# Performance work log

Measured on AMD Instinct MI355X. Metric: run time of the kernel, lower is better.

## Reference

```python
import jax, jax.numpy as jnp
import numpy as np

B, N, D = 8, 4096, 512
K = 1228  # int(4096 * 0.3)
N_CH = 2


def setup_inputs() -> dict:
    key = jax.random.key(0)
    ks = jax.random.split(key, 6)
    return {
        "agents_states": jax.random.normal(ks[0], (B, N, D), jnp.float32),
        "net": jax.random.normal(ks[1], (N_CH, N, N), jnp.float32) * (1.0 / np.sqrt(N)),
        "gate_w": jax.random.normal(ks[2], (N_CH, D, 2 * D), jnp.float32) * 0.02,
        "gate_b": jnp.zeros((N_CH, D), jnp.float32),
        "cand_w": jax.random.normal(ks[3], (N_CH, D, D), jnp.float32) * 0.02,
        "cand_b": jnp.zeros((N_CH, D), jnp.float32),
        "ln_g": jnp.ones((N_CH, D), jnp.float32),
        "ln_b": jnp.zeros((N_CH, D), jnp.float32),
        "channel_mix": jnp.ones((N_CH,), jnp.float32) / N_CH,
        "k": K,
    }


def _layer_norm(h, g, b, eps=1e-5):
    mu = h.mean(-1, keepdims=True)
    var = jnp.mean((h - mu) ** 2, axis=-1, keepdims=True)
    return (h - mu) * jax.lax.rsqrt(var + eps) * g + b


def _channel(x, net, gw, gb, cw, cb, lg, lb):
    # fixed-graph message passing: [N,N] @ [B,N,D]
    interaction = jnp.einsum('mn,bnd->bmd', net, x)
    candidate = jax.nn.gelu(interaction @ cw.T + cb, approximate=False)
    gate = jax.nn.sigmoid(jnp.concatenate([x, interaction], axis=-1) @ gw.T + gb)
    return _layer_norm(gate * candidate + (1.0 - gate) * x, lg, lb)


def reference(agents_states, net, gate_w, gate_b, cand_w, cand_b, ln_g, ln_b, channel_mix, k):
    w = jax.nn.softmax(channel_mix, axis=0)
    out = jnp.zeros_like(agents_states)
    for c in range(net.shape[0]):  # fixed small channel count
        out = out + w[c] * _channel(agents_states, net[c], gate_w[c], gate_b[c],
                                    cand_w[c], cand_b[c], ln_g[c], ln_b[c])
    # sparse top-k activation over agents
    energy = jnp.linalg.norm(out, axis=-1)               # [B, N]
    _, top_idx = jax.lax.top_k(energy, k)                # [B, k]
    mask = jnp.zeros_like(energy).at[jnp.arange(energy.shape[0])[:, None], top_idx].set(1.0)
    mask = mask * (out.shape[1] / k)
    return out * mask[..., None]
```

## Files before the change

### kernel.cpp

```cpp
#include <hip/hip_runtime.h>
#include <hip/hip_bf16.h>
#include <math.h>

#define BB 8
#define NN 4096
#define DD 512
#define SLAB 2048
#define SROWS (BB * SLAB)

typedef short bf16x8 __attribute__((ext_vector_type(8)));
typedef float f32x4 __attribute__((ext_vector_type(4)));

#define AS1 __attribute__((address_space(1)))
#define AS3 __attribute__((address_space(3)))

__device__ __forceinline__ void gload_lds16(const void* g, void* l) {
    __builtin_amdgcn_global_load_lds((const AS1 unsigned int*)g,
                                     (AS3 unsigned int*)l, 16, 0, 0);
}

__device__ __forceinline__ void split_bf16(float v, unsigned short& h, unsigned short& l) {
    __hip_bfloat16 bh = __float2bfloat16(v);
    float hf = __bfloat162float(bh);
    __hip_bfloat16 bl = __float2bfloat16(v - hf);
    h = *reinterpret_cast<unsigned short*>(&bh);
    l = *reinterpret_cast<unsigned short*>(&bl);
}

__global__ __launch_bounds__(256)
void conv_split(const float* __restrict__ src, unsigned short* __restrict__ hi,
                unsigned short* __restrict__ lo)
{
    const size_t i = (size_t)blockIdx.x * 256 + threadIdx.x;
    float4 v = ((const float4*)src)[i];
    ushort4 h, l;
    split_bf16(v.x, h.x, l.x);
    split_bf16(v.y, h.y, l.y);
    split_bf16(v.z, h.z, l.z);
    split_bf16(v.w, h.w, l.w);
    ((ushort4*)hi)[i] = h;
    ((ushort4*)lo)[i] = l;
}

__global__ __launch_bounds__(256)
void conv_w3(const float* __restrict__ cw, const float* __restrict__ gw,
             unsigned short* __restrict__ cwh, unsigned short* __restrict__ cwl,
             unsigned short* __restrict__ gxh, unsigned short* __restrict__ gxl,
             unsigned short* __restrict__ gih, unsigned short* __restrict__ gil)
{
    const int blk = blockIdx.x;
    const int i = (blk & 255) * 256 + threadIdx.x;
    const int n = i >> 7, kq = (i & 127) * 4;
    const float* src;
    unsigned short *oh, *ol;
    if (blk < 256)      { src = cw + (size_t)n * 512 + kq;        oh = cwh; ol = cwl; }
    else if (blk < 512) { src = gw + (size_t)n * 1024 + kq;       oh = gxh; ol = gxl; }
    else                { src = gw + (size_t)n * 1024 + 512 + kq; oh = gih; ol = gil; }
    float4 v = *(const float4*)src;
    ushort4 h, l;
    split_bf16(v.x, h.x, l.x);
    split_bf16(v.y, h.y, l.y);
    split_bf16(v.z, h.z, l.z);
    split_bf16(v.w, h.w, l.w);
    *(ushort4*)(oh + (size_t)n * 512 + kq) = h;
    *(ushort4*)(ol + (size_t)n * 512 + kq) = l;
}

__global__ __launch_bounds__(256)
void conv_xs(const float* __restrict__ x, int nbase,
             unsigned short* __restrict__ hi, unsigned short* __restrict__ lo)
{
    const size_t i = (size_t)blockIdx.x * 256 + threadIdx.x;
    const int r = (int)(i >> 7), kq = (int)(i & 127) * 4;
    const int b = r >> 11, ii = r & (SLAB - 1);
    float4 v = *(const float4*)(x + ((size_t)(b << 12) + nbase + ii) * DD + kq);
    ushort4 h, l;
    split_bf16(v.x, h.x, l.x);
    split_bf16(v.y, h.y, l.y);
    split_bf16(v.z, h.z, l.z);
    split_bf16(v.w, h.w, l.w);
    *(ushort4*)(hi + (size_t)r * DD + kq) = h;
    *(ushort4*)(lo + (size_t)r * DD + kq) = l;
}

__global__ __launch_bounds__(256)
void conv_xT(const float* __restrict__ x, unsigned short* __restrict__ th,
             unsigned short* __restrict__ tl)
{
    __shared__ unsigned short Th[64][65];
    __shared__ unsigned short Tl[64][65];
    const int n0 = blockIdx.x * 64, d0 = blockIdx.y * 64, b = blockIdx.z;
    const int t = threadIdx.x;
    const int r = t >> 4, c4 = (t & 15) * 4;
#pragma unroll
    for (int i = 0; i < 4; ++i) {
        int row = r + i * 16;
        float4 v = *(const float4*)(x + ((size_t)b * NN + n0 + row) * DD + d0 + c4);
        split_bf16(v.x, Th[row][c4 + 0], Tl[row][c4 + 0]);
        split_bf16(v.y, Th[row][c4 + 1], Tl[row][c4 + 1]);
        split_bf16(v.z, Th[row][c4 + 2], Tl[row][c4 + 2]);
        split_bf16(v.w, Th[row][c4 + 3], Tl[row][c4 + 3]);
    }
    __syncthreads();
    const int od = t >> 2;
    const int on0 = (t & 3) * 16;
    unsigned short hb[16], lb[16];
#pragma unroll
    for (int j = 0; j < 16; ++j) { hb[j] = Th[on0 + j][od]; lb[j] = Tl[on0 + j][od]; }
    const size_t obase = ((size_t)b * DD + d0 + od) * (size_t)NN + n0 + on0;
#pragma unroll
    for (int q = 0; q < 4; ++q) {
        ushort4 hv = {hb[q * 4 + 0], hb[q * 4 + 1], hb[q * 4 + 2], hb[q * 4 + 3]};
        ushort4 lv = {lb[q * 4 + 0], lb[q * 4 + 1], lb[q * 4 + 2], lb[q * 4 + 3]};
        *(ushort4*)(th + obase + q * 4) = hv;
        *(ushort4*)(tl + obase + q * 4) = lv;
    }
}

__global__ __launch_bounds__(256, 2)
void gemm_big(const unsigned short* __restrict__ Ah, const unsigned short* __restrict__ Al,
              const unsigned short* __restrict__ Bh, const unsigned short* __restrict__ Bl,
              unsigned short* __restrict__ Ch, unsigned short* __restrict__ Cl)
{
    __shared__ alignas(16) unsigned short sAh[2][128 * 32];
    __shared__ alignas(16) unsigned short sAl[2][128 * 32];
    __shared__ alignas(16) unsigned short sBh[2][128 * 32];
    __shared__ alignas(16) unsigned short sBl[2][128 * 32];

    const int tid = threadIdx.x;
    const int lane = tid & 63;
    const int w = tid >> 6;

    const int lin = blockIdx.x + (blockIdx.y << 2) + (blockIdx.z << 5);
    const int swz = (lin & 7) * 64 + (lin >> 3);
    const int n0 = (swz & 3) * 128;
    const int b  = (swz >> 2) & 7;
    const int m0 = (swz >> 5) * 128;

    Bh += (size_t)b * DD * NN;
    Bl += (size_t)b * DD * NN;

    const int c0 = w * 2, c1 = c0 + 1;
    const int u2 = lane >> 2;
    const int sst = (u2 + (u2 >> 2)) & 3;
    const int kc = (lane & 3) ^ sst;
    const size_t gA0 = (size_t)(m0 + c0 * 16 + u2) * NN + kc * 8;
    const size_t gA1 = (size_t)(m0 + c1 * 16 + u2) * NN + kc * 8;
    const size_t gB0 = (size_t)(n0 + c0 * 16 + u2) * NN + kc * 8;
    const size_t gB1 = (size_t)(n0 + c1 * 16 + u2) * NN + kc * 8;

    auto stage = [&](int buf, int koff) {
        unsigned short* bAh = sAh[buf];
        unsigned short* bAl = sAl[buf];
        unsigned short* bBh = sBh[buf];
        unsigned short* bBl = sBl[buf];
        gload_lds16(Ah + gA0 + koff, bAh + c0 * 512);
        gload_lds16(Ah + gA1 + koff, bAh + c1 * 512);
        gload_lds16(Al + gA0 + koff, bAl + c0 * 512);
        gload_lds16(Al + gA1 + koff, bAl + c1 * 512);
        gload_lds16(Bh + gB0 + koff, bBh + c0 * 512);
        gload_lds16(Bh + gB1 + koff, bBh + c1 * 512);
        gload_lds16(Bl + gB0 + koff, bBl + c0 * 512);
        gload_lds16(Bl + gB1 + koff, bBl + c1 * 512);
    };

    const int wm = (w & 1) * 64, wn = (w >> 1) * 64;
    const int fr = lane & 15;
    const int sf = (fr + (fr >> 2)) & 3;
    const int fslot = ((lane >> 4) ^ sf) * 16;
    int offA[4], offB[4];
#pragma unroll
    for (int i = 0; i < 4; ++i) {
        offA[i] = (wm + i * 16 + fr) * 64 + fslot;
        offB[i] = (wn + i * 16 + fr) * 64 + fslot;
    }

    f32x4 acc[4][4] = {};

    stage(0, 0);
    asm volatile("s_waitcnt vmcnt(0)" ::: "memory");
    __syncthreads();

    int cur = 0;
    for (int kt = 0; kt < NN; kt += 32) {
        if (kt + 32 < NN) stage(cur ^ 1, kt + 32);

        bf16x8 ah[4], al[4], bh[4], bl[4];
#pragma unroll
        for (int i = 0; i < 4; ++i) {
            ah[i] = *(const bf16x8*)((const char*)sAh[cur] + offA[i]);
            al[i] = *(const bf16x8*)((const char*)sAl[cur] + offA[i]);
            bh[i] = *(const bf16x8*)((const char*)sBh[cur] + offB[i]);
            bl[i] = *(const bf16x8*)((const char*)sBl[cur] + offB[i]);
        }
#pragma unroll
        for (int mi = 0; mi < 4; ++mi)
#pragma unroll
            for (int ni = 0; ni < 4; ++ni) {
                acc[mi][ni] = __builtin_amdgcn_mfma_f32_16x16x32_bf16(al[mi], bh[ni], acc[mi][ni], 0, 0, 0);
                acc[mi][ni] = __builtin_amdgcn_mfma_f32_16x16x32_bf16(ah[mi], bl[ni], acc[mi][ni], 0, 0, 0);
                acc[mi][ni] = __builtin_amdgcn_mfma_f32_16x16x32_bf16(ah[mi], bh[ni], acc[mi][ni], 0, 0, 0);
            }

        asm volatile("s_waitcnt vmcnt(0)" ::: "memory");
        __syncthreads();
        cur ^= 1;
    }

    const int erow = (lane >> 4) * 4;
#pragma unroll
    for (int mi = 0; mi < 4; ++mi)
#pragma unroll
        for (int ni = 0; ni < 4; ++ni) {
            const int r0 = m0 + wm + mi * 16 + erow;
            const int col = n0 + wn + ni * 16 + fr;
#pragma unroll
            for (int r = 0; r < 4; ++r) {
                unsigned short h, l;
                split_bf16(acc[mi][ni][r], h, l);
                const size_t idx = ((size_t)b * SLAB + r0 + r) * DD + col;
                Ch[idx] = h;
                Cl[idx] = l;
            }
        }
}

__global__ __launch_bounds__(256, 2)
void gemm_small(const unsigned short* __restrict__ Ah, const unsigned short* __restrict__ Al,
                const unsigned short* __restrict__ Bh, const unsigned short* __restrict__ Bl,
                const float* __restrict__ bias, float* __restrict__ C, int accum)
{
    __shared__ alignas(16) unsigned short sAh[2][128 * 32];
    __shared__ alignas(16) unsigned short sAl[2][128 * 32];
    __shared__ alignas(16) unsigned short sBh[2][128 * 32];
    __shared__ alignas(16) unsigned short sBl[2][128 * 32];

    const int tid = threadIdx.x;
    const int lane = tid & 63;
    const int w = tid >> 6;

    const int lin = blockIdx.x + (blockIdx.y << 2);
    const int swz = (lin & 7) * 64 + (lin >> 3);
    const int n0 = (swz & 3) * 128;
    const int m0 = (swz >> 2) * 128;

    const int c0 = w * 2, c1 = c0 + 1;
    const int u2 = lane >> 2;
    const int sst = (u2 + (u2 >> 2)) & 3;
    const int kc = (lane & 3) ^ sst;
    const size_t gA0 = (size_t)(m0 + c0 * 16 + u2) * DD + kc * 8;
    const size_t gA1 = (size_t)(m0 + c1 * 16 + u2) * DD + kc * 8;
    const size_t gB0 = (size_t)(n0 + c0 * 16 + u2) * DD + kc * 8;
    const size_t gB1 = (size_t)(n0 + c1 * 16 + u2) * DD + kc * 8;

    auto stage = [&](int buf, int koff) {
        unsigned short* bAh = sAh[buf];
        unsigned short* bAl = sAl[buf];
        unsigned short* bBh = sBh[buf];
        unsigned short* bBl = sBl[buf];
        gload_lds16(Ah + gA0 + koff, bAh + c0 * 512);
        gload_lds16(Ah + gA1 + koff, bAh + c1 * 512);
        gload_lds16(Al + gA0 + koff, bAl + c0 * 512);
        gload_lds16(Al + gA1 + koff, bAl + c1 * 512);
        gload_lds16(Bh + gB0 + koff, bBh + c0 * 512);
        gload_lds16(Bh + gB1 + koff, bBh + c1 * 512);
        gload_lds16(Bl + gB0 + koff, bBl + c0 * 512);
        gload_lds16(Bl + gB1 + koff, bBl + c1 * 512);
    };

    const int wm = (w & 1) * 64, wn = (w >> 1) * 64;
    const int fr = lane & 15;
    const int sf = (fr + (fr >> 2)) & 3;
    const int fslot = ((lane >> 4) ^ sf) * 16;
    int offA[4], offB[4];
#pragma unroll
    for (int i = 0; i < 4; ++i) {
        offA[i] = (wm + i * 16 + fr) * 64 + fslot;
        offB[i] = (wn + i * 16 + fr) * 64 + fslot;
    }

    f32x4 acc[4][4] = {};

    stage(0, 0);
    asm volatile("s_waitcnt vmcnt(0)" ::: "memory");
    __syncthreads();

    int cur = 0;
    for (int kt = 0; kt < DD; kt += 32) {
        if (kt + 32 < DD) stage(cur ^ 1, kt + 32);

        bf16x8 ah[4], al[4], bh[4], bl[4];
#pragma unroll
        for (int i = 0; i < 4; ++i) {
            ah[i] = *(const bf16x8*)((const char*)sAh[cur] + offA[i]);
            al[i] = *(const bf16x8*)((const char*)sAl[cur] + offA[i]);
            bh[i] = *(const bf16x8*)((const char*)sBh[cur] + offB[i]);
            bl[i] = *(const bf16x8*)((const char*)sBl[cur] + offB[i]);
        }
#pragma unroll
        for (int mi = 0; mi < 4; ++mi)
#pragma unroll
            for (int ni = 0; ni < 4; ++ni) {
                acc[mi][ni] = __builtin_amdgcn_mfma_f32_16x16x32_bf16(al[mi], bh[ni], acc[mi][ni], 0, 0, 0);
                acc[mi][ni] = __builtin_amdgcn_mfma_f32_16x16x32_bf16(ah[mi], bl[ni], acc[mi][ni], 0, 0, 0);
                acc[mi][ni] = __builtin_amdgcn_mfma_f32_16x16x32_bf16(ah[mi], bh[ni], acc[mi][ni], 0, 0, 0);
            }

        asm volatile("s_waitcnt vmcnt(0)" ::: "memory");
        __syncthreads();
        cur ^= 1;
    }

    const int erow = (lane >> 4) * 4;
#pragma unroll
    for (int mi = 0; mi < 4; ++mi)
#pragma unroll
        for (int ni = 0; ni < 4; ++ni) {
            const int r0 = m0 + wm + mi * 16 + erow;
            const int col = n0 + wn + ni * 16 + fr;
            const float bv = bias ? bias[col] : 0.0f;
#pragma unroll
            for (int r = 0; r < 4; ++r) {
                const size_t idx = (size_t)(r0 + r) * DD + col;
                float v = acc[mi][ni][r] + bv;
                if (accum) v += C[idx];
                C[idx] = v;
            }
        }
}

__global__ __launch_bounds__(128)
void pw_slab(const float* __restrict__ x, const float* __restrict__ gp_,
             const float* __restrict__ cp_, const float* __restrict__ lg,
             const float* __restrict__ lb, const float* __restrict__ cmix,
             int c, int nbase, float* __restrict__ out, float* __restrict__ energy)
{
    __shared__ float sm[4];
    const int rloc = blockIdx.x;
    const int b = rloc >> 11, ii = rloc & (SLAB - 1);
    const int grow = (b << 12) + nbase + ii;
    const int tid = threadIdx.x;
    const size_t lbase = (size_t)rloc * DD + tid * 4;
    const size_t gbase = (size_t)grow * DD + tid * 4;

    float4 g4 = *(const float4*)(gp_ + lbase);
    float4 c4 = *(const float4*)(cp_ + lbase);
    float4 x4 = *(const float4*)(x + gbase);
    float gv[4] = {g4.x, g4.y, g4.z, g4.w};
    float cv[4] = {c4.x, c4.y, c4.z, c4.w};
    float xv[4] = {x4.x, x4.y, x4.z, x4.w};
    float h[4];
#pragma unroll
    for (int j = 0; j < 4; ++j) {
        float gate = 1.0f / (1.0f + expf(-gv[j]));
        float cand = 0.5f * cv[j] * (1.0f + erff(cv[j] * 0.70710678118654752440f));
        h[j] = gate * cand + (1.0f - gate) * xv[j];
    }

    const int lane = tid & 63, wid = tid >> 6;
    float s = h[0] + h[1] + h[2] + h[3];
#pragma unroll
    for (int off = 32; off > 0; off >>= 1) s += __shfl_xor(s, off, 64);
    if (lane == 0) sm[wid] = s;
    __syncthreads();
    float mu = (sm[0] + sm[1]) * (1.0f / 512.0f);
    float vs = 0.0f;
#pragma unroll
    for (int j = 0; j < 4; ++j) { float d = h[j] - mu; vs += d * d; }
#pragma unroll
    for (int off = 32; off > 0; off >>= 1) vs += __shfl_xor(vs, off, 64);
    if (lane == 0) sm[2 + wid] = vs;
    __syncthreads();
    float var = (sm[2] + sm[3]) * (1.0f / 512.0f);
    float rstd = 1.0f / sqrtf(var + 1e-5f);

    float m0 = cmix[0], m1 = cmix[1];
    float mx = fmaxf(m0, m1);
    float e0 = expf(m0 - mx), e1 = expf(m1 - mx);
    float wgt = ((c == 0) ? e0 : e1) / (e0 + e1);

    const int dix = tid * 4;
    float4 lg4 = *(const float4*)(lg + dix);
    float4 lb4 = *(const float4*)(lb + dix);
    float lgv[4] = {lg4.x, lg4.y, lg4.z, lg4.w};
    float lbv[4] = {lb4.x, lb4.y, lb4.z, lb4.w};
    float ov[4];
    if (c == 0) {
#pragma unroll
        for (int j = 0; j < 4; ++j)
            ov[j] = wgt * ((h[j] - mu) * rstd * lgv[j] + lbv[j]);
    } else {
        float4 o4 = *(const float4*)(out + gbase);
        ov[0] = o4.x; ov[1] = o4.y; ov[2] = o4.z; ov[3] = o4.w;
#pragma unroll
        for (int j = 0; j < 4; ++j)
            ov[j] += wgt * ((h[j] - mu) * rstd * lgv[j] + lbv[j]);
    }
    float4 st = {ov[0], ov[1], ov[2], ov[3]};
    *(float4*)(out + gbase) = st;

    if (c == 1) {
        float s2 = ov[0] * ov[0] + ov[1] * ov[1] + ov[2] * ov[2] + ov[3] * ov[3];
#pragma unroll
        for (int off = 32; off > 0; off >>= 1) s2 += __shfl_xor(s2, off, 64);
        __syncthreads();
        if (lane == 0) sm[wid] = s2;
        __syncthreads();
        if (tid == 0) energy[grow] = sqrtf(sm[0] + sm[1]);
    }
}

__global__ __launch_bounds__(1024)
void topk_kernel(float* __restrict__ energy, const int* __restrict__ kptr)
{
    __shared__ unsigned keys[NN];
    __shared__ int hist[256];
    __shared__ int wsum[16];
    __shared__ unsigned sh_pfx;
    __shared__ int sh_need;

    const int b = blockIdx.x, tid = threadIdx.x;
    float* e = energy + (size_t)b * NN;
    for (int n = tid; n < NN; n += 1024) keys[n] = __float_as_uint(e[n]);
    const int K = *kptr;
    if (tid == 0) { sh_pfx = 0u; sh_need = K; }
    __syncthreads();

    for (int round = 0; round < 4; ++round) {
        const int shift = 24 - 8 * round;
        if (tid < 256) hist[tid] = 0;
        __syncthreads();
        const unsigned pfx = sh_pfx;
        const unsigned mhi = (round == 0) ? 0u : (0xFFFFFFFFu << (shift + 8));
        for (int n = tid; n < NN; n += 1024) {
            unsigned kv = keys[n];
            if ((kv & mhi) == pfx) atomicAdd(&hist[(kv >> shift) & 255], 1);
        }
        __syncthreads();
        if (tid == 0) {
            int need = sh_need;
            int d = 255;
            for (;; --d) {
                int cct = hist[d];
                if (need <= cct) break;
                need -= cct;
            }
            sh_pfx = pfx | ((unsigned)d << shift);
            sh_need = need;
        }
        __syncthreads();
    }

    const unsigned T = sh_pfx;
    const int need = sh_need;

    const int n0 = tid * 4;
    unsigned kv[4]; int eq[4]; int loc[4];
    int s = 0;
#pragma unroll
    for (int j = 0; j < 4; ++j) {
        kv[j] = keys[n0 + j];
        eq[j] = (kv[j] == T) ? 1 : 0;
        loc[j] = s; s += eq[j];
    }
    const int lane = tid & 63, wid = tid >> 6;
    int v = s;
#pragma unroll
    for (int off = 1; off < 64; off <<= 1) {
        int u = __shfl_up(v, off, 64);
        if (lane >= off) v += u;
    }
    if (lane == 63) wsum[wid] = v;
    __syncthreads();
    if (tid == 0) {
        int acc = 0;
        for (int w2 = 0; w2 < 16; ++w2) { int t = wsum[w2]; wsum[w2] = acc; acc += t; }
    }
    __syncthreads();
    const int base = wsum[wid] + (v - s);
    const float scale = (float)(4096.0 / (double)K);
#pragma unroll
    for (int j = 0; j < 4; ++j) {
        bool sel = (kv[j] > T) || (eq[j] && (base + loc[j]) < need);
        e[n0 + j] = sel ? scale : 0.0f;
    }
}

__global__ __launch_bounds__(128)
void mask_kernel(float* __restrict__ out, const float* __restrict__ mscale)
{
    const int row = blockIdx.x;
    const int tid = threadIdx.x;
    const size_t base = (size_t)row * DD + tid * 4;
    const float sc = mscale[row];
    float4 v = *(const float4*)(out + base);
    v.x *= sc; v.y *= sc; v.z *= sc; v.w *= sc;
    *(float4*)(out + base) = v;
}

extern "C" void kernel_launch(void* const* d_in, const int* in_sizes, int n_in,
                              void* d_out, int out_size, void* d_ws, size_t ws_size,
                              hipStream_t stream)
{
    const float* x      = (const float*)d_in[0];
    const float* net    = (const float*)d_in[1];
    const float* gate_w = (const float*)d_in[2];
    const float* gate_b = (const float*)d_in[3];
    const float* cand_w = (const float*)d_in[4];
    const float* cand_b = (const float*)d_in[5];
    const float* ln_g   = (const float*)d_in[6];
    const float* ln_b   = (const float*)d_in[7];
    const float* cmix   = (const float*)d_in[8];
    const int*   kptr   = (const int*)d_in[9];
    float* out = (float*)d_out;

    const size_t ROWS  = (size_t)BB * NN;
    const size_t PLANE = ROWS * DD;

    char* p = (char*)d_ws;
    unsigned short* xTh = (unsigned short*)p;             p += PLANE * 2;
    unsigned short* xTl = (unsigned short*)p;             p += PLANE * 2;
    char* slotN = p;                                      p += (size_t)SLAB * NN * 2 * 2;
    unsigned short* netsh = (unsigned short*)slotN;
    unsigned short* netsl = netsh + (size_t)SLAB * NN;
    unsigned short* cwh = (unsigned short*)slotN;
    unsigned short* cwl = cwh + 512 * 512;
    unsigned short* gxh = cwl + 512 * 512;
    unsigned short* gxl = gxh + 512 * 512;
    unsigned short* gih = gxl + 512 * 512;
    unsigned short* gil = gih + 512 * 512;
    unsigned short* inth = (unsigned short*)p;            p += (size_t)SROWS * DD * 2;
    unsigned short* intl = (unsigned short*)p;            p += (size_t)SROWS * DD * 2;
    char* slotX = p;                                      p += (size_t)SROWS * DD * 4;
    unsigned short* xsh = (unsigned short*)slotX;
    unsigned short* xsl = xsh + (size_t)SROWS * DD;
    float* candp = (float*)slotX;
    float* gatep = (float*)p;                             p += (size_t)SROWS * DD * 4;
    float* energy = (float*)p;

    conv_xT<<<dim3(NN / 64, DD / 64, BB), 256, 0, stream>>>(x, xTh, xTl);

    for (int c = 0; c < 2; ++c) {
        for (int s = 0; s < 2; ++s) {
            const int nbase = s * SLAB;
            conv_split<<<(SLAB * NN / 4) / 256, 256, 0, stream>>>(
                net + (size_t)c * NN * NN + (size_t)nbase * NN, netsh, netsl);
            gemm_big<<<dim3(DD / 128, BB, SLAB / 128), 256, 0, stream>>>(
                netsh, netsl, xTh, xTl, inth, intl);
            conv_w3<<<768, 256, 0, stream>>>(
                cand_w + (size_t)c * DD * DD, gate_w + (size_t)c * DD * 2 * DD,
                cwh, cwl, gxh, gxl, gih, gil);
            conv_xs<<<(SROWS * DD / 4) / 256, 256, 0, stream>>>(x, nbase, xsh, xsl);
            gemm_small<<<dim3(4, SROWS / 128), 256, 0, stream>>>(
                xsh, xsl, gxh, gxl, gate_b + (size_t)c * DD, gatep, 0);
            gemm_small<<<dim3(4, SROWS / 128), 256, 0, stream>>>(
                inth, intl, cwh, cwl, cand_b + (size_t)c * DD, candp, 0);
            gemm_small<<<dim3(4, SROWS / 128), 256, 0, stream>>>(
                inth, intl, gih, gil, nullptr, gatep, 1);
            pw_slab<<<SROWS, 128, 0, stream>>>(
                x, gatep, candp, ln_g + (size_t)c * DD, ln_b + (size_t)c * DD,
                cmix, c, nbase, out, energy);
        }
    }

    topk_kernel<<<BB, 1024, 0, stream>>>(energy, kptr);
    mask_kernel<<<(int)ROWS, 128, 0, stream>>>(out, energy);
}
```

Baseline: 1.782 ms.

## Fuse candidate and gate GEMMs sharing interaction input; single-buffer LDS in GEMMs

Adds a dual-output GEMM kernel that loads the interaction tile once and multiplies it by both the gate-interaction weights and the candidate weights, replacing two separate launches that each reread the interaction matrix. It also converts all GEMM kernels from double-buffered LDS prefetch to a single buffer with load, wait and sync inside each k-step. This halves LDS use per block and may raise occupancy, but it removes the overlap of global loads with MFMA work, which can stall the large GEMM. The fused kernel holds two accumulator sets, which raises register pressure.

```diff
diff --git a/kernel.cpp b/kernel.cpp
--- a/kernel.cpp
+++ b/kernel.cpp
@@ -122,10 +122,10 @@
               const unsigned short* __restrict__ Bh, const unsigned short* __restrict__ Bl,
               unsigned short* __restrict__ Ch, unsigned short* __restrict__ Cl)
 {
-    __shared__ alignas(16) unsigned short sAh[2][128 * 32];
-    __shared__ alignas(16) unsigned short sAl[2][128 * 32];
-    __shared__ alignas(16) unsigned short sBh[2][128 * 32];
-    __shared__ alignas(16) unsigned short sBl[2][128 * 32];
+    __shared__ alignas(16) unsigned short sAh[128 * 32];
+    __shared__ alignas(16) unsigned short sAl[128 * 32];
+    __shared__ alignas(16) unsigned short sBh[128 * 32];
+    __shared__ alignas(16) unsigned short sBl[128 * 32];
 
     const int tid = threadIdx.x;
     const int lane = tid & 63;
@@ -148,21 +148,10 @@
     const size_t gA1 = (size_t)(m0 + c1 * 16 + u2) * NN + kc * 8;
     const size_t gB0 = (size_t)(n0 + c0 * 16 + u2) * NN + kc * 8;
     const size_t gB1 = (size_t)(n0 + c1 * 16 + u2) * NN + kc * 8;
-
-    auto stage = [&](int buf, int koff) {
-        unsigned short* bAh = sAh[buf];
-        unsigned short* bAl = sAl[buf];
-        unsigned short* bBh = sBh[buf];
-        unsigned short* bBl = sBl[buf];
-        gload_lds16(Ah + gA0 + koff, bAh + c0 * 512);
-        gload_lds16(Ah + gA1 + koff, bAh + c1 * 512);
-        gload_lds16(Al + gA0 + koff, bAl + c0 * 512);
-        gload_lds16(Al + gA1 + koff, bAl + c1 * 512);
-        gload_lds16(Bh + gB0 + koff, bBh + c0 * 512);
-        gload_lds16(Bh + gB1 + koff, bBh + c1 * 512);
-        gload_lds16(Bl + gB0 + koff, bBl + c0 * 512);
-        gload_lds16(Bl + gB1 + koff, bBl + c1 * 512);
-    };
+    unsigned short* lAh0 = sAh + c0 * 512; unsigned short* lAh1 = sAh + c1 * 512;
+    unsigned short* lAl0 = sAl + c0 * 512; unsigned short* lAl1 = sAl + c1 * 512;
+    unsigned short* lBh0 = sBh + c0 * 512; unsigned short* lBh1 = sBh + c1 * 512;
+    unsigned short* lBl0 = sBl + c0 * 512; unsigned short* lBl1 = sBl + c1 * 512;
 
     const int wm = (w & 1) * 64, wn = (w >> 1) * 64;
     const int fr = lane & 15;
@@ -177,21 +166,26 @@
 
     f32x4 acc[4][4] = {};
 
-    stage(0, 0);
-    asm volatile("s_waitcnt vmcnt(0)" ::: "memory");
-    __syncthreads();
-
-    int cur = 0;
     for (int kt = 0; kt < NN; kt += 32) {
-        if (kt + 32 < NN) stage(cur ^ 1, kt + 32);
+        __syncthreads();
+        gload_lds16(Ah + gA0 + kt, lAh0);
+        gload_lds16(Ah + gA1 + kt, lAh1);
+        gload_lds16(Al + gA0 + kt, lAl0);
+        gload_lds16(Al + gA1 + kt, lAl1);
+        gload_lds16(Bh + gB0 + kt, lBh0);
+        gload_lds16(Bh + gB1 + kt, lBh1);
+        gload_lds16(Bl + gB0 + kt, lBl0);
+        gload_lds16(Bl + gB1 + kt, lBl1);
+        asm volatile("s_waitcnt vmcnt(0)" ::: "memory");
+        __syncthreads();
 
         bf16x8 ah[4], al[4], bh[4], bl[4];
 #pragma unroll
         for (int i = 0; i < 4; ++i) {
-            ah[i] = *(const bf16x8*)((const char*)sAh[cur] + offA[i]);
-            al[i] = *(const bf16x8*)((const char*)sAl[cur] + offA[i]);
-            bh[i] = *(const bf16x8*)((const char*)sBh[cur] + offB[i]);
-            bl[i] = *(const bf16x8*)((const char*)sBl[cur] + offB[i]);
+            ah[i] = *(const bf16x8*)((const char*)sAh + offA[i]);
+            al[i] = *(const bf16x8*)((const char*)sAl + offA[i]);
+            bh[i] = *(const bf16x8*)((const char*)sBh + offB[i]);
+            bl[i] = *(const bf16x8*)((const char*)sBl + offB[i]);
         }
 #pragma unroll
         for (int mi = 0; mi < 4; ++mi)
@@ -201,10 +195,6 @@
                 acc[mi][ni] = __builtin_amdgcn_mfma_f32_16x16x32_bf16(ah[mi], bl[ni], acc[mi][ni], 0, 0, 0);
                 acc[mi][ni] = __builtin_amdgcn_mfma_f32_16x16x32_bf16(ah[mi], bh[ni], acc[mi][ni], 0, 0, 0);
             }
-
-        asm volatile("s_waitcnt vmcnt(0)" ::: "memory");
-        __syncthreads();
-        cur ^= 1;
     }
 
     const int erow = (lane >> 4) * 4;
@@ -230,10 +220,10 @@
                 const unsigned short* __restrict__ Bh, const unsigned short* __restrict__ Bl,
                 const float* __restrict__ bias, float* __restrict__ C, int accum)
 {
-    __shared__ alignas(16) unsigned short sAh[2][128 * 32];
-    __shared__ alignas(16) unsigned short sAl[2][128 * 32];
-    __shared__ alignas(16) unsigned short sBh[2][128 * 32];
-    __shared__ alignas(16) unsigned short sBl[2][128 * 32];
+    __shared__ alignas(16) unsigned short sAh[128 * 32];
+    __shared__ alignas(16) unsigned short sAl[128 * 32];
+    __shared__ alignas(16) unsigned short sBh[128 * 32];
+    __shared__ alignas(16) unsigned short sBl[128 * 32];
 
     const int tid = threadIdx.x;
     const int lane = tid & 63;
@@ -252,21 +242,10 @@
     const size_t gA1 = (size_t)(m0 + c1 * 16 + u2) * DD + kc * 8;
     const size_t gB0 = (size_t)(n0 + c0 * 16 + u2) * DD + kc * 8;
     const size_t gB1 = (size_t)(n0 + c1 * 16 + u2) * DD + kc * 8;
-
-    auto stage = [&](int buf, int koff) {
-        unsigned short* bAh = sAh[buf];
-        unsigned short* bAl = sAl[buf];
-        unsigned short* bBh = sBh[buf];
-        unsigned short* bBl = sBl[buf];
-        gload_lds16(Ah + gA0 + koff, bAh + c0 * 512);
-        gload_lds16(Ah + gA1 + koff, bAh + c1 * 512);
-        gload_lds16(Al + gA0 + koff, bAl + c0 * 512);
-        gload_lds16(Al + gA1 + koff, bAl + c1 * 512);
-        gload_lds16(Bh + gB0 + koff, bBh + c0 * 512);
-        gload_lds16(Bh + gB1 + koff, bBh + c1 * 512);
-        gload_lds16(Bl + gB0 + koff, bBl + c0 * 512);
-        gload_lds16(Bl + gB1 + koff, bBl + c1 * 512);
-    };
+    unsigned short* lAh0 = sAh + c0 * 512; unsigned short* lAh1 = sAh + c1 * 512;
+    unsigned short* lAl0 = sAl + c0 * 512; unsigned short* lAl1 = sAl + c1 * 512;
+    unsigned short* lBh0 = sBh + c0 * 512; unsigned short* lBh1 = sBh + c1 * 512;
+    unsigned short* lBl0 = sBl + c0 * 512; unsigned short* lBl1 = sBl + c1 * 512;
 
     const int wm = (w & 1) * 64, wn = (w >> 1) * 64;
     const int fr = lane & 15;
@@ -281,21 +260,26 @@
 
     f32x4 acc[4][4] = {};
 
-    stage(0, 0);
-    asm volatile("s_waitcnt vmcnt(0)" ::: "memory");
-    __syncthreads();
-
-    int cur = 0;
     for (int kt = 0; kt < DD; kt += 32) {
-        if (kt + 32 < DD) stage(cur ^ 1, kt + 32);
+        __syncthreads();
+        gload_lds16(Ah + gA0 + kt, lAh0);
+        gload_lds16(Ah + gA1 + kt, lAh1);
+        gload_lds16(Al + gA0 + kt, lAl0);
+        gload_lds16(Al + gA1 + kt, lAl1);
+        gload_lds16(Bh + gB0 + kt, lBh0);
+        gload_lds16(Bh + gB1 + kt, lBh1);
+        gload_lds16(Bl + gB0 + kt, lBl0);
+        gload_lds16(Bl + gB1 + kt, lBl1);
+        asm volatile("s_waitcnt vmcnt(0)" ::: "memory");
+        __syncthreads();
 
         bf16x8 ah[4], al[4], bh[4], bl[4];
 #pragma unroll
         for (int i = 0; i < 4; ++i) {
-            ah[i] = *(const bf16x8*)((const char*)sAh[cur] + offA[i]);
-            al[i] = *(const bf16x8*)((const char*)sAl[cur] + offA[i]);
-            bh[i] = *(const bf16x8*)((const char*)sBh[cur] + offB[i]);
-            bl[i] = *(const bf16x8*)((const char*)sBl[cur] + offB[i]);
+            ah[i] = *(const bf16x8*)((const char*)sAh + offA[i]);
+            al[i] = *(const bf16x8*)((const char*)sAl + offA[i]);
+            bh[i] = *(const bf16x8*)((const char*)sBh + offB[i]);
+            bl[i] = *(const bf16x8*)((const char*)sBl + offB[i]);
         }
 #pragma unroll
         for (int mi = 0; mi < 4; ++mi)
@@ -305,10 +289,6 @@
                 acc[mi][ni] = __builtin_amdgcn_mfma_f32_16x16x32_bf16(ah[mi], bl[ni], acc[mi][ni], 0, 0, 0);
                 acc[mi][ni] = __builtin_amdgcn_mfma_f32_16x16x32_bf16(ah[mi], bh[ni], acc[mi][ni], 0, 0, 0);
             }
-
-        asm volatile("s_waitcnt vmcnt(0)" ::: "memory");
-        __syncthreads();
-        cur ^= 1;
     }
 
     const int erow = (lane >> 4) * 4;
@@ -325,6 +305,120 @@
                 float v = acc[mi][ni][r] + bv;
                 if (accum) v += C[idx];
                 C[idx] = v;
+            }
+        }
+}
+
+__global__ __launch_bounds__(256, 2)
+void gemm_small_dual(const unsigned short* __restrict__ Ah, const unsigned short* __restrict__ Al,
+                     const unsigned short* __restrict__ Gh, const unsigned short* __restrict__ Gl,
+                     const unsigned short* __restrict__ Wh, const unsigned short* __restrict__ Wl,
+                     const float* __restrict__ cbias, float* __restrict__ gatep,
+                     float* __restrict__ candp)
+{
+    __shared__ alignas(16) unsigned short sAh[128 * 32];
+    __shared__ alignas(16) unsigned short sAl[128 * 32];
+    __shared__ alignas(16) unsigned short sGh[128 * 32];
+    __shared__ alignas(16) unsigned short sGl[128 * 32];
+    __shared__ alignas(16) unsigned short sWh[128 * 32];
+    __shared__ alignas(16) unsigned short sWl[128 * 32];
+
+    const int tid = threadIdx.x;
+    const int lane = tid & 63;
+    const int w = tid >> 6;
+
+    const int lin = blockIdx.x + (blockIdx.y << 2);
+    const int swz = (lin & 7) * 64 + (lin >> 3);
+    const int n0 = (swz & 3) * 128;
+    const int m0 = (swz >> 2) * 128;
+
+    const int c0 = w * 2, c1 = c0 + 1;
+    const int u2 = lane >> 2;
+    const int sst = (u2 + (u2 >> 2)) & 3;
+    const int kc = (lane & 3) ^ sst;
+    const size_t gA0 = (size_t)(m0 + c0 * 16 + u2) * DD + kc * 8;
+    const size_t gA1 = (size_t)(m0 + c1 * 16 + u2) * DD + kc * 8;
+    const size_t gB0 = (size_t)(n0 + c0 * 16 + u2) * DD + kc * 8;
+    const size_t gB1 = (size_t)(n0 + c1 * 16 + u2) * DD + kc * 8;
+
+    const int wm = (w & 1) * 64, wn = (w >> 1) * 64;
+    const int fr = lane & 15;
+    const int sf = (fr + (fr >> 2)) & 3;
+    const int fslot = ((lane >> 4) ^ sf) * 16;
+    int offA[4], offB[4];
+#pragma unroll
+    for (int i = 0; i < 4; ++i) {
+        offA[i] = (wm + i * 16 + fr) * 64 + fslot;
+        offB[i] = (wn + i * 16 + fr) * 64 + fslot;
+    }
+
+    f32x4 accG[4][4] = {};
+    f32x4 accC[4][4] = {};
+
+    for (int kt = 0; kt < DD; kt += 32) {
+        __syncthreads();
+        gload_lds16(Ah + gA0 + kt, sAh + c0 * 512);
+        gload_lds16(Ah + gA1 + kt, sAh + c1 * 512);
+        gload_lds16(Al + gA0 + kt, sAl + c0 * 512);
+        gload_lds16(Al + gA1 + kt, sAl + c1 * 512);
+        gload_lds16(Gh + gB0 + kt, sGh + c0 * 512);
+        gload_lds16(Gh + gB1 + kt, sGh + c1 * 512);
+        gload_lds16(Gl + gB0 + kt, sGl + c0 * 512);
+        gload_lds16(Gl + gB1 + kt, sGl + c1 * 512);
+        gload_lds16(Wh + gB0 + kt, sWh + c0 * 512);
+        gload_lds16(Wh + gB1 + kt, sWh + c1 * 512);
+        gload_lds16(Wl + gB0 + kt, sWl + c0 * 512);
+        gload_lds16(Wl + gB1 + kt, sWl + c1 * 512);
+        asm volatile("s_waitcnt vmcnt(0)" ::: "memory");
+        __syncthreads();
+
+        bf16x8 ah[4], al[4], bh[4], bl[4];
+#pragma unroll
+        for (int i = 0; i < 4; ++i) {
+            ah[i] = *(const bf16x8*)((const char*)sAh + offA[i]);
+            al[i] = *(const bf16x8*)((const char*)sAl + offA[i]);
+        }
+#pragma unroll
+        for (int i = 0; i < 4; ++i) {
+            bh[i] = *(const bf16x8*)((const char*)sGh + offB[i]);
+            bl[i] = *(const bf16x8*)((const char*)sGl + offB[i]);
+        }
+#pragma unroll
+        for (int mi = 0; mi < 4; ++mi)
+#pragma unroll
+            for (int ni = 0; ni < 4; ++ni) {
+                accG[mi][ni] = __builtin_amdgcn_mfma_f32_16x16x32_bf16(al[mi], bh[ni], accG[mi][ni], 0, 0, 0);
+                accG[mi][ni] = __builtin_amdgcn_mfma_f32_16x16x32_bf16(ah[mi], bl[ni], accG[mi][ni], 0, 0, 0);
+                accG[mi][ni] = __builtin_amdgcn_mfma_f32_16x16x32_bf16(ah[mi], bh[ni], accG[mi][ni], 0, 0, 0);
+            }
+#pragma unroll
+        for (int i = 0; i < 4; ++i) {
+            bh[i] = *(const bf16x8*)((const char*)sWh + offB[i]);
+            bl[i] = *(const bf16x8*)((const char*)sWl + offB[i]);
+        }
+#pragma unroll
+        for (int mi = 0; mi < 4; ++mi)
+#pragma unroll
+            for (int ni = 0; ni < 4; ++ni) {
+                accC[mi][ni] = __builtin_amdgcn_mfma_f32_16x16x32_bf16(al[mi], bh[ni], accC[mi][ni], 0, 0, 0);
+                accC[mi][ni] = __builtin_amdgcn_mfma_f32_16x16x32_bf16(ah[mi], bl[ni], accC[mi][ni], 0, 0, 0);
+                accC[mi][ni] = __builtin_amdgcn_mfma_f32_16x16x32_bf16(ah[mi], bh[ni], accC[mi][ni], 0, 0, 0);
+            }
+    }
+
+    const int erow = (lane >> 4) * 4;
+#pragma unroll
+    for (int mi = 0; mi < 4; ++mi)
+#pragma unroll
+        for (int ni = 0; ni < 4; ++ni) {
+            const int r0 = m0 + wm + mi * 16 + erow;
+            const int col = n0 + wn + ni * 16 + fr;
+            const float cb = cbias[col];
+#pragma unroll
+            for (int r = 0; r < 4; ++r) {
+                const size_t idx = (size_t)(r0 + r) * DD + col;
+                gatep[idx] += accG[mi][ni][r];
+                candp[idx] = accC[mi][ni][r] + cb;
             }
         }
 }
@@ -553,10 +647,8 @@
             conv_xs<<<(SROWS * DD / 4) / 256, 256, 0, stream>>>(x, nbase, xsh, xsl);
             gemm_small<<<dim3(4, SROWS / 128), 256, 0, stream>>>(
                 xsh, xsl, gxh, gxl, gate_b + (size_t)c * DD, gatep, 0);
-            gemm_small<<<dim3(4, SROWS / 128), 256, 0, stream>>>(
-                inth, intl, cwh, cwl, cand_b + (size_t)c * DD, candp, 0);
-            gemm_small<<<dim3(4, SROWS / 128), 256, 0, stream>>>(
-                inth, intl, gih, gil, nullptr, gatep, 1);
+            gemm_small_dual<<<dim3(4, SROWS / 128), 256, 0, stream>>>(
+                inth, intl, gih, gil, cwh, cwl, cand_b + (size_t)c * DD, gatep, candp);
             pw_slab<<<SROWS, 128, 0, stream>>>(
                 x, gatep, candp, ln_g + (size_t)c * DD, ln_b + (size_t)c * DD,
                 cmix, c, nbase, out, energy);
```

After: 1.690 ms. 1.05x faster.
